# Performance work log

Measured on AMD Instinct MI355X. Metric: run time of the kernel, lower is better.

Reference implementation:

```python
import jax, jax.numpy as jnp
import numpy as np

NUM_SUB = (128, 32)
NUM_NEI = (24, 24)
LN_EPS = 1e-5


def bilinear(fmap, pts):
    # fmap: [C,H,W]; pts: [P,2] as (y,x) normalized to [0,1]; align_corners=True
    C, H, W = fmap.shape
    gy = pts[:, 0] * (H - 1)
    gx = pts[:, 1] * (W - 1)
    y0 = jnp.floor(gy)
    x0 = jnp.floor(gx)
    wy = gy - y0
    wx = gx - x0
    y0i = jnp.clip(y0.astype(jnp.int32), 0, H - 1)
    y1i = jnp.clip(y0i + 1, 0, H - 1)
    x0i = jnp.clip(x0.astype(jnp.int32), 0, W - 1)
    x1i = jnp.clip(x0i + 1, 0, W - 1)
    v00 = fmap[:, y0i, x0i]
    v01 = fmap[:, y0i, x1i]
    v10 = fmap[:, y1i, x0i]
    v11 = fmap[:, y1i, x1i]
    out = (v00 * (1 - wy) * (1 - wx) + v01 * (1 - wy) * wx
           + v10 * wy * (1 - wx) + v11 * wy * wx)
    return out.T  # [P,C]


def fps(xyz, npoint):
    # farthest point sampling, deterministic start at index 0. xyz: [B,N,2]
    B, N, _ = xyz.shape
    bidx = jnp.arange(B)

    def step(carry, _):
        dist, far = carry
        c = xyz[bidx, far][:, None, :]            # [B,1,2]
        d = jnp.sum((xyz - c) ** 2, -1)           # [B,N]
        dist = jnp.minimum(dist, d)
        return (dist, jnp.argmax(dist, -1)), far

    init = (jnp.full((B, N), 1e10, xyz.dtype), jnp.zeros((B,), jnp.int32))
    _, idx = jax.lax.scan(step, init, None, length=npoint)
    return idx.T  # [B,npoint]


def sqdist(a, b):
    # a: [B,S,2], b: [B,N,2] -> [B,S,N]
    return (jnp.sum(a ** 2, -1)[..., None] + jnp.sum(b ** 2, -1)[:, None, :]
            - 2.0 * jnp.einsum('bsc,bnc->bsn', a, b))


def layernorm(x, g, b):
    m = jnp.mean(x, -1, keepdims=True)
    v = jnp.mean((x - m) ** 2, -1, keepdims=True)
    return (x - m) / jnp.sqrt(v + LN_EPS) * g + b


def setup_inputs() -> dict:
    key = jax.random.key(0)
    ks = jax.random.split(key, 8)
    B, N, C, H, W = 32, 512, 1024, 24, 24
    Dp = C + 2
    out_dim = 4096
    return {
        'feature_map': jax.random.normal(ks[0], (B, C, H, W), jnp.float32),
        'points': jax.random.uniform(ks[1], (B, N, 2), jnp.float32),
        'W_diff': jax.random.normal(ks[2], (2, Dp, Dp), jnp.float32) * 0.02,
        'b_diff': jnp.zeros((2, Dp), jnp.float32),
        'W_agg': jax.random.normal(ks[3], (2, C, 2 * Dp), jnp.float32) * 0.02,
        'b_agg': jnp.zeros((2, C), jnp.float32),
        'ln_g': jnp.ones((2, C), jnp.float32),
        'ln_b': jnp.zeros((2, C), jnp.float32),
        'W_flat': jax.random.normal(ks[4], (C, C * NUM_SUB[-1]), jnp.float32) * 0.02,
        'b_flat': jnp.zeros((C,), jnp.float32),
        'W_dim': jax.random.normal(ks[5], (out_dim, C), jnp.float32) * 0.02,
        'b_dim': jnp.zeros((out_dim,), jnp.float32),
    }


def reference(feature_map, points, W_diff, b_diff, W_agg, b_agg,
              ln_g, ln_b, W_flat, b_flat, W_dim, b_dim):
    B = points.shape[0]
    all_pts = points                              # [B,N,2]
    all_fea = jax.vmap(bilinear)(feature_map, points)  # [B,N,C]
    bidx = jnp.arange(B)[:, None, None]
    for i, (S, K) in enumerate(zip(NUM_SUB, NUM_NEI)):
        fi = fps(all_pts, S)                                   # [B,S]
        new_pts = jnp.take_along_axis(all_pts, fi[..., None], 1)   # [B,S,2]
        new_fea = jnp.take_along_axis(all_fea, fi[..., None], 1)   # [B,S,C]
        d2 = sqdist(new_pts, all_pts)                          # [B,S,N]
        _, idx = jax.lax.top_k(-d2, K)                         # [B,S,K]
        grp_pts = all_pts[bidx, idx]                           # [B,S,K,2]
        grp_fea = all_fea[bidx, idx]                           # [B,S,K,C]
        local = jnp.concatenate([grp_fea, grp_pts], -1)        # [B,S,K,C+2]
        anchor = jnp.concatenate([new_fea, new_pts], -1)[:, :, None, :]
        diff = jnp.einsum('bskd,od->bsko', local - anchor, W_diff[i]) + b_diff[i]
        gath = jnp.concatenate([diff, jnp.broadcast_to(anchor, diff.shape)], -1)
        # Conv1d(kernel=1) + ReLU + LayerNorm over channels
        h = jax.nn.relu(jnp.einsum('bskd,od->bsko', gath, W_agg[i]) + b_agg[i])
        h = layernorm(h, ln_g[i], ln_b[i])
        all_pts, all_fea = new_pts, jnp.mean(h, 2)             # mean pool over K
    x = all_fea.reshape(B, -1)
    x = x @ W_flat.T + b_flat
    return x @ W_dim.T + b_dim
```

## Files before the change

### kernel.cpp

```cpp
#include <hip/hip_runtime.h>


typedef float f32x4 __attribute__((ext_vector_type(4)));
typedef short bf16x8 __attribute__((ext_vector_type(8)));
typedef unsigned short u16;
typedef u16 u16x4 __attribute__((ext_vector_type(4)));
typedef unsigned int u32;
typedef u32 u32x4 __attribute__((ext_vector_type(4)));
typedef unsigned long long u64;

typedef const void __attribute__((address_space(1)))* gvp;
typedef void __attribute__((address_space(3)))* svp;

__device__ __forceinline__ u16 f2bf(float f) {
  union { float f; u32 u; } x; x.f = f;
  u32 r = x.u + 0x7fffu + ((x.u >> 16) & 1u);
  return (u16)(r >> 16);
}

#define KP 1056
#define NP0 1152

__device__ __forceinline__ float rl_f(float v, int lane) {
  return __int_as_float(__builtin_amdgcn_readlane(__float_as_int(v), lane));
}

template <int CTRL>
__device__ __forceinline__ float dpp_fmax(float v) {
  float o = __int_as_float(__builtin_amdgcn_update_dpp(
      (int)0xff800000 , __float_as_int(v), CTRL, 0xf, 0xf, false));
  return fmaxf(v, o);
}

template <int CTRL>
__device__ __forceinline__ float dpp_fmin(float v) {
  float o = __int_as_float(__builtin_amdgcn_update_dpp(
      0x7f800000 , __float_as_int(v), CTRL, 0xf, 0xf, false));
  return fminf(v, o);
}

template <int CTRL>
__device__ __forceinline__ float dpp_add(float v) {
  float o = __int_as_float(__builtin_amdgcn_update_dpp(
      0, __float_as_int(v), CTRL, 0xf, 0xf, false));
  return v + o;
}

__device__ __forceinline__ float wave_fmax63(float v) {
  v = dpp_fmax<0x111>(v);
  v = dpp_fmax<0x112>(v);
  v = dpp_fmax<0x114>(v);
  v = dpp_fmax<0x118>(v);
  v = dpp_fmax<0x142>(v);
  v = dpp_fmax<0x143>(v);
  return rl_f(v, 63);
}

__device__ __forceinline__ float wave_fmin63(float v) {
  v = dpp_fmin<0x111>(v);
  v = dpp_fmin<0x112>(v);
  v = dpp_fmin<0x114>(v);
  v = dpp_fmin<0x118>(v);
  v = dpp_fmin<0x142>(v);
  v = dpp_fmin<0x143>(v);
  return rl_f(v, 63);
}

__device__ __forceinline__ float wave_sum63(float v) {
  v = dpp_add<0x111>(v);
  v = dpp_add<0x112>(v);
  v = dpp_add<0x114>(v);
  v = dpp_add<0x118>(v);
  v = dpp_add<0x142>(v);
  v = dpp_add<0x143>(v);
  return v;
}

template <int PPL, int HS>
__device__ void fps_core(const float* __restrict__ pts, int* __restrict__ fi,
                         float* __restrict__ npts,
                         int Np, int S, int b, int lane, int s0, int s1,
                         float* __restrict__ dsave, int* __restrict__ fsave) {
  #pragma clang fp contract(off)
  float px[PPL], py[PPL], dist[PPL];
  #pragma unroll
  for (int j = 0; j < PPL; ++j) {
    int n = j * 64 + lane;
    px[j] = pts[((size_t)b * Np + n) * 2];
    py[j] = pts[((size_t)b * Np + n) * 2 + 1];
  }
  int far; float cx, cy;
  if (s0 == 0) {
    #pragma unroll
    for (int j = 0; j < PPL; ++j) dist[j] = 1e10f;
    far = 0;
    cx = rl_f(px[0], 0);
    cy = rl_f(py[0], 0);
  } else {
    #pragma unroll
    for (int j = 0; j < PPL; ++j) dist[j] = dsave[(size_t)b * Np + j * 64 + lane];
    far = fsave[b];
    cx = pts[((size_t)b * Np + far) * 2];
    cy = pts[((size_t)b * Np + far) * 2 + 1];
  }
  int hist[HS];
  #pragma unroll
  for (int h = 0; h < HS; ++h) hist[h] = 0;
  for (int s = s0; s < s1; ++s) {
    #pragma unroll
    for (int h = 0; h < HS; ++h)
      if ((s >> 6) == h && (s & 63) == lane) hist[h] = far;
    float tv[PPL]; int ti[PPL]; float tx[PPL], ty[PPL];
    #pragma unroll
    for (int j = 0; j < PPL; ++j) {
      float dx = px[j] - cx, dy = py[j] - cy;
      float d = dx * dx + dy * dy;
      float nd = fminf(dist[j], d);
      dist[j] = nd;
      tv[j] = nd; ti[j] = j * 64 + lane; tx[j] = px[j]; ty[j] = py[j];
    }
    #pragma unroll
    for (int w = PPL; w > 1; w >>= 1)
      #pragma unroll
      for (int j = 0; j < (w >> 1); ++j)
        if (tv[j + (w >> 1)] > tv[j]) {
          tv[j] = tv[j + (w >> 1)]; ti[j] = ti[j + (w >> 1)];
          tx[j] = tx[j + (w >> 1)]; ty[j] = ty[j + (w >> 1)];
        }
    float smax = wave_fmax63(tv[0]);
    u64 mask = __ballot(tv[0] == smax);
    int L = __builtin_ctzll(mask);
    int fidx = __builtin_amdgcn_readlane(ti[0], L);
    float fx = rl_f(tx[0], L), fy = rl_f(ty[0], L);
    u64 rest = mask & (mask - 1);
    if (__builtin_expect(rest != 0, 0)) {
      while (rest) {
        int L2 = __builtin_ctzll(rest);
        int c = __builtin_amdgcn_readlane(ti[0], L2);
        if (c < fidx) {
          fidx = c; fx = rl_f(tx[0], L2); fy = rl_f(ty[0], L2);
        }
        rest &= rest - 1;
      }
    }
    far = fidx; cx = fx; cy = fy;
  }
  if (s1 < S) {
    #pragma unroll
    for (int j = 0; j < PPL; ++j) dsave[(size_t)b * Np + j * 64 + lane] = dist[j];
    if (lane == 0) fsave[b] = far;
  }
  #pragma unroll
  for (int h = 0; h < HS; ++h) {
    int s = h * 64 + lane;
    if (s >= s0 && s < s1) {
      int hv = hist[h];
      fi[b * S + s] = hv;
      npts[(size_t)(b * S + s) * 2]     = pts[((size_t)b * Np + hv) * 2];
      npts[(size_t)(b * S + s) * 2 + 1] = pts[((size_t)b * Np + hv) * 2 + 1];
    }
  }
}

template <int PPL>
__device__ void knn_core(const float* __restrict__ qpts,
                         const float* __restrict__ rpts,
                         int* __restrict__ idxK, int Np, int S, int q, int lane) {
  #pragma clang fp contract(off)
  int b = q / S;
  float ax = qpts[(size_t)q * 2], ay = qpts[(size_t)q * 2 + 1];
  float a2 = ax * ax + ay * ay;
  float d2[PPL];
  #pragma unroll
  for (int j = 0; j < PPL; ++j) {
    int n = j * 64 + lane;
    float bx = rpts[((size_t)b * Np + n) * 2];
    float by = rpts[((size_t)b * Np + n) * 2 + 1];
    float b2 = bx * bx + by * by;
    float dot = ax * bx + ay * by;
    float t = a2 + b2;
    float m2 = 2.f * dot;
    d2[j] = t - m2;
  }
  int kreg = 0;
  for (int k = 0; k < 24; ++k) {
    float tv[PPL]; int ti[PPL];
    #pragma unroll
    for (int j = 0; j < PPL; ++j) { tv[j] = d2[j]; ti[j] = j * 64 + lane; }
    #pragma unroll
    for (int w = PPL; w > 1; w >>= 1)
      #pragma unroll
      for (int j = 0; j < (w >> 1); ++j)
        if (tv[j + (w >> 1)] < tv[j]) {
          tv[j] = tv[j + (w >> 1)]; ti[j] = ti[j + (w >> 1)];
        }
    float smin = wave_fmin63(tv[0]);
    u64 mask = __ballot(tv[0] == smin);
    int L = __builtin_ctzll(mask);
    int bs = __builtin_amdgcn_readlane(ti[0], L);
    u64 rest = mask & (mask - 1);
    if (__builtin_expect(rest != 0, 0)) {
      while (rest) {
        int L2 = __builtin_ctzll(rest);
        int c = __builtin_amdgcn_readlane(ti[0], L2);
        if (c < bs) bs = c;
        rest &= rest - 1;
      }
    }
    if (lane == k) kreg = bs;
    #pragma unroll
    for (int j = 0; j < PPL; ++j)
      if (j * 64 + lane == bs) d2[j] = 3.4e38f;
  }
  if (lane < 24) idxK[(size_t)q * 24 + lane] = kreg;
}

template <int BF16OUT, int IND>
__device__ __forceinline__ void gemm_tile_body(const u16* __restrict__ A,
                                               const u16* __restrict__ Bt,
                                               void* __restrict__ Cout,
                                               int K, int ldc, int nvalid,
                                               int m0, int n0,
                                               const int* __restrict__ find,
                                               int iNp, int iS,
                                               u16* __restrict__ As,
                                               u16* __restrict__ Bs) {
  const int tid = threadIdx.x;
  const int lane = tid & 63;
  const int wv = tid >> 6;
  const int wm = (wv >> 1) * 64;
  const int wn = (wv & 1) * 64;

  f32x4 acc[4][4];
  #pragma unroll
  for (int i = 0; i < 4; ++i)
    #pragma unroll
    for (int j = 0; j < 4; ++j)
      #pragma unroll
      for (int c = 0; c < 4; ++c) acc[i][j][c] = 0.f;

  const int ch0 = wv * 2;
  const int rin = lane >> 2;
  const int slot = lane & 3;
  const int cin = (slot ^ (rin & 3) ^ ((rin >> 2) & 3)) * 8;

  size_t aro[2];
  #pragma unroll
  for (int i = 0; i < 2; ++i) {
    const int row = (ch0 + i) * 16 + rin;
    if (IND) {
      const int q = m0 + row;
      aro[i] = (size_t)(q / iS) * iNp + find[q];
    } else {
      aro[i] = (size_t)(m0 + row);
    }
  }

  for (int k0 = 0; k0 < K; k0 += 32) {
    #pragma unroll
    for (int i = 0; i < 2; ++i) {
      const int ch = ch0 + i;
      const int row = ch * 16 + rin;
      const u16* ga = A + aro[i] * K + (k0 + cin);
      const u16* gb = Bt + (size_t)(n0 + row) * K + (k0 + cin);
      __builtin_amdgcn_global_load_lds((gvp)ga, (svp)(As + ch * 512), 16, 0, 0);
      __builtin_amdgcn_global_load_lds((gvp)gb, (svp)(Bs + ch * 512), 16, 0, 0);
    }
    __syncthreads();
    const int rf = lane & 15;
    const int quad = lane >> 4;
    const int qs = (quad ^ (rf & 3) ^ ((rf >> 2) & 3)) * 8;
    bf16x8 af[4], bfv[4];
    #pragma unroll
    for (int mi = 0; mi < 4; ++mi)
      af[mi] = *(const bf16x8*)(As + (wm + mi * 16 + rf) * 32 + qs);
    #pragma unroll
    for (int ni = 0; ni < 4; ++ni)
      bfv[ni] = *(const bf16x8*)(Bs + (wn + ni * 16 + rf) * 32 + qs);
    #pragma unroll
    for (int mi = 0; mi < 4; ++mi)
      #pragma unroll
      for (int ni = 0; ni < 4; ++ni)
        acc[mi][ni] = __builtin_amdgcn_mfma_f32_16x16x32_bf16(af[mi], bfv[ni], acc[mi][ni], 0, 0, 0);
    __syncthreads();
  }

  const int rq = (lane >> 4) * 4;
  const int cf = lane & 15;
  #pragma unroll
  for (int mi = 0; mi < 4; ++mi) {
    #pragma unroll
    for (int ni = 0; ni < 4; ++ni) {
      const int col = n0 + wn + ni * 16 + cf;
      #pragma unroll
      for (int r = 0; r < 4; ++r) {
        const int row = m0 + wm + mi * 16 + rq + r;
        const float v = acc[mi][ni][r];
        if (BF16OUT) {
          if (col < nvalid) ((u16*)Cout)[(size_t)row * ldc + col] = f2bf(v);
        } else {
          ((float*)Cout)[(size_t)row * ldc + col] = v;
        }
      }
    }
  }
}

__global__ __launch_bounds__(256, 2) void bilinear_fused_kernel(const float* __restrict__ fmap,
                                                                const float* __restrict__ pts,
                                                                u16* __restrict__ X,
                                                                int* __restrict__ fi0,
                                                                float* __restrict__ npts0,
                                                                float* __restrict__ fdist,
                                                                int* __restrict__ ffar) {
  if (blockIdx.y == 0) {
    if (blockIdx.x < 8)
      fps_core<8, 2>(pts, fi0, npts0, 512, 128, blockIdx.x * 4 + (threadIdx.x >> 6),
                     threadIdx.x & 63, 0, 32, fdist, ffar);
    return;
  }
  __shared__ float fmS[32][580];
  const int ct = blockIdx.x, b = blockIdx.y - 1;
  const int t = threadIdx.x;
  const float* src = fmap + ((size_t)b * 1024 + ct * 32) * 576;
  const int tr = t >> 3, ti = t & 7;
  #pragma unroll
  for (int j = 0; j < 18; ++j) {
    int c4 = j * 8 + ti;
    *(f32x4*)&fmS[tr][c4 * 4] = *(const f32x4*)(src + (size_t)tr * 576 + c4 * 4);
  }
  __syncthreads();
  #pragma unroll
  for (int pass = 0; pass < 2; ++pass) {
    const int n = pass * 256 + t;
    const int pidx = b * 512 + n;
    float p0 = pts[(size_t)pidx * 2], p1 = pts[(size_t)pidx * 2 + 1];
    float gy = p0 * 23.f, gx = p1 * 23.f;
    float y0f = floorf(gy), x0f = floorf(gx);
    float wy = gy - y0f, wx = gx - x0f;
    int y0 = (int)y0f; y0 = y0 < 0 ? 0 : (y0 > 23 ? 23 : y0);
    int x0 = (int)x0f; x0 = x0 < 0 ? 0 : (x0 > 23 ? 23 : x0);
    int y1 = y0 + 1 > 23 ? 23 : y0 + 1;
    int x1 = x0 + 1 > 23 ? 23 : x0 + 1;
    float w00 = (1.f - wy) * (1.f - wx), w01 = (1.f - wy) * wx;
    float w10 = wy * (1.f - wx), w11 = wy * wx;
    const int i00 = y0 * 24 + x0, i01 = y0 * 24 + x1;
    const int i10 = y1 * 24 + x0, i11 = y1 * 24 + x1;
    size_t ro = (size_t)pidx * KP + ct * 32;
    #pragma unroll
    for (int cq = 0; cq < 8; ++cq) {
      u16x4 o4;
      #pragma unroll
      for (int cc = 0; cc < 4; ++cc) {
        int c = cq * 4 + cc;
        float v = w00 * fmS[c][i00] + w01 * fmS[c][i01] +
                  w10 * fmS[c][i10] + w11 * fmS[c][i11];
        o4[cc] = f2bf(v);
      }
      *(u16x4*)(X + ro + cq * 4) = o4;
    }
    if (ct == 31) {
      size_t rb = (size_t)pidx * KP;
      X[rb + 1024] = f2bf(p0);
      X[rb + 1025] = f2bf(p1);
      #pragma unroll
      for (int z = 0; z < 15; ++z) ((u32*)(X + rb + 1026))[z] = 0;
    }
  }
}

__global__ __launch_bounds__(256) void wd_transpose_kernel(const float* __restrict__ Wd,
                                                           u16* __restrict__ WdT) {
  __shared__ float tbuf[32][33];
  const float* Wds = Wd + (size_t)blockIdx.z * 1026 * 1026;
  u16* WdTs = WdT + (size_t)blockIdx.z * NP0 * KP;
  int tx = threadIdx.x & 31, ty = threadIdx.x >> 5;
  int ot = blockIdx.x * 32, dt = blockIdx.y * 32;
  #pragma unroll
  for (int j = 0; j < 4; ++j) {
    int o = ot + ty + 8 * j, d = dt + tx;
    tbuf[ty + 8 * j][tx] = (o < 1026 && d < 1026) ? Wds[(size_t)o * 1026 + d] : 0.f;
  }
  __syncthreads();
  #pragma unroll
  for (int j = 0; j < 4; ++j) {
    int d = dt + ty + 8 * j, o = ot + tx;
    if (o < KP) WdTs[(size_t)d * KP + o] = f2bf(tbuf[tx][ty + 8 * j]);
  }
}

__global__ __launch_bounds__(256) void waggcz_kernel(const float* __restrict__ Wagg,
                                                     const float* __restrict__ bdiff,
                                                     const float* __restrict__ bagg,
                                                     u16* __restrict__ Wa1,
                                                     u16* __restrict__ Wa2,
                                                     float* __restrict__ czero) {
  __shared__ float red[4];
  const int bid = blockIdx.x;
  const int stage = bid >> 10, c = bid & 1023;
  const float* row = Wagg + (size_t)stage * 1024 * 2052 + (size_t)c * 2052;
  const float* bd = bdiff + stage * 1026;
  u16* wa1 = Wa1 + (size_t)stage * 1024 * KP + (size_t)c * KP;
  u16* wa2 = Wa2 + (size_t)stage * 1024 * KP + (size_t)c * KP;
  const int t = threadIdx.x;
  float acc = 0.f;
  for (int d = t; d < KP; d += 256) {
    if (d < 1026) {
      float v1 = row[d];
      float v2 = row[1026 + d];
      wa1[d] = f2bf(v1);
      wa2[d] = f2bf(v2);
      acc += bd[d] * v1;
    } else {
      wa1[d] = 0;
      wa2[d] = 0;
    }
  }
  float s = wave_sum63(acc);
  const int lane = t & 63, wv = t >> 6;
  if (lane == 63) red[wv] = s;
  __syncthreads();
  if (t == 0)
    czero[(size_t)stage * 1024 + c] = red[0] + red[1] + red[2] + red[3] + bagg[stage * 1024 + c];
}

__global__ __launch_bounds__(256) void wcomb_dual_kernel(const u16* __restrict__ Wa1,
                                                         const u16* __restrict__ WdT,
                                                         u16* __restrict__ Wcomb,
                                                         const float* __restrict__ fpts,
                                                         int* __restrict__ ffi,
                                                         float* __restrict__ fnpts,
                                                         float* __restrict__ fdist,
                                                         int* __restrict__ ffar) {
  __shared__ __align__(16) u16 As[128 * 32];
  __shared__ __align__(16) u16 Bs[128 * 32];
  const int wv = threadIdx.x >> 6, lane = threadIdx.x & 63;
  if (blockIdx.y == 0) {
    if (blockIdx.x < 8)
      fps_core<8, 2>(fpts, ffi, fnpts, 512, 128, blockIdx.x * 4 + wv, lane, 32, 56,
                     fdist, ffar);
    return;
  }
  const int y = blockIdx.y - 1;
  const int stage = y >> 3;
  const int mt = y & 7;
  const u16* A = Wa1 + (size_t)stage * 1024 * KP;
  const u16* B = WdT + (size_t)stage * NP0 * KP;
  u16* C = Wcomb + (size_t)stage * 1024 * KP;
  gemm_tile_body<1, 0>(A, B, C, KP, KP, KP, mt * 128, blockIdx.x * 128,
                       nullptr, 0, 0, As, Bs);
}

template <int BF16OUT, int FPS_PPL, int FPS_HS, int SWZ, int KNN_PPL, int IND>
__global__ __launch_bounds__(256) void gemm_bt_kernel(const u16* __restrict__ A,
                                                      const u16* __restrict__ Bt,
                                                      void* __restrict__ Cout,
                                                      int K, int ldc, int nvalid,
                                                      const int* __restrict__ find,
                                                      int iNp, int iS,
                                                      const float* __restrict__ fpts,
                                                      int* __restrict__ ffi,
                                                      float* __restrict__ fnpts,
                                                      int fNp, int fS, int fs0, int fs1,
                                                      float* __restrict__ fdist,
                                                      int* __restrict__ ffar,
                                                      const float* __restrict__ kq,
                                                      const float* __restrict__ kr,
                                                      int* __restrict__ kidx,
                                                      int kNp, int kS, int kYoff) {
  const int tid = threadIdx.x;
  const int lane = tid & 63;
  const int wv = tid >> 6;
  const int FR = (FPS_PPL > 0) ? 1 : 0;
  if (FPS_PPL > 0 && blockIdx.y == 0) {
    if (blockIdx.x < 8)
      fps_core<FPS_PPL ? FPS_PPL : 1, FPS_HS>(fpts, ffi, fnpts, fNp, fS,
                                              blockIdx.x * 4 + wv, lane, fs0, fs1,
                                              fdist, ffar);
    return;
  }
  if (KNN_PPL > 0 && (int)blockIdx.y >= kYoff) {
    int kb = ((int)blockIdx.y - kYoff) * gridDim.x + blockIdx.x;
    knn_core<KNN_PPL ? KNN_PPL : 1>(kq, kr, kidx, kNp, kS, kb * 4 + wv, lane);
    return;
  }
  __shared__ __align__(16) u16 As[128 * 32];
  __shared__ __align__(16) u16 Bs[128 * 32];
  int mt, nt;
  if (SWZ) {
    const int g = ((int)blockIdx.y - FR) * gridDim.x + blockIdx.x;
    const int MT = (KNN_PPL > 0 ? kYoff : (int)gridDim.y) - FR;
    const int cpx = MT >> 3;
    const int xcd = g & 7;
    const int r = g >> 3;
    mt = xcd * cpx + (r >> 3);
    nt = r & 7;
  } else {
    mt = (int)blockIdx.y - FR;
    nt = blockIdx.x;
  }
  gemm_tile_body<BF16OUT, IND>(A, Bt, Cout, K, ldc, nvalid, mt * 128, nt * 128,
                               find, iNp, iS, As, Bs);
}

template <int MODE, int FPS_PPL, int FPS_HS>
__global__ __launch_bounds__(256) void h_epilogue_kernel(const float* __restrict__ Z1,
                                                         const float* __restrict__ Z2g,
                                                         const float* __restrict__ czero,
                                                         const int* __restrict__ idxK,
                                                         const int* __restrict__ fi,
                                                         const float* __restrict__ g,
                                                         const float* __restrict__ bb,
                                                         const float* __restrict__ npts,
                                                         void* __restrict__ outp,
                                                         int Np, int S, int cpx,
                                                         const float* __restrict__ fpts,
                                                         int* __restrict__ ffi,
                                                         float* __restrict__ fnpts,
                                                         int fNp, int fS) {
  const int t = threadIdx.x;
  const int lane = t & 63, wv = t >> 6;
  if (FPS_PPL > 0 && blockIdx.x < 8) {
    fps_core<FPS_PPL ? FPS_PPL : 1, FPS_HS>(fpts, ffi, fnpts, fNp, fS,
                                            blockIdx.x * 4 + wv, lane, 0, fS,
                                            nullptr, nullptr);
    return;
  }
  const int bid = blockIdx.x - (FPS_PPL > 0 ? 8 : 0);
  const int sw = (bid & 7) * cpx + (bid >> 3);
  const int q = sw * 4 + wv;
  const int b = q / S;
  const int fiv = fi[q];
  const float* z2 = Z2g + (size_t)q * 1024;
  const float* zf = Z1 + ((size_t)b * Np + fiv) * 1024;
  const int ch = lane * 4;

  f32x4 base[4], gv[4], bv[4], acc[4];
  #pragma unroll
  for (int j = 0; j < 4; ++j) {
    f32x4 a = *(const f32x4*)(z2 + j * 256 + ch);
    f32x4 c = *(const f32x4*)(czero + j * 256 + ch);
    f32x4 f = *(const f32x4*)(zf + j * 256 + ch);
    #pragma unroll
    for (int c2 = 0; c2 < 4; ++c2) base[j][c2] = a[c2] + c[c2] - f[c2];
    gv[j] = *(const f32x4*)(g + j * 256 + ch);
    bv[j] = *(const f32x4*)(bb + j * 256 + ch);
    #pragma unroll
    for (int c2 = 0; c2 < 4; ++c2) acc[j][c2] = 0.f;
  }
  int nk = 0;
  if (lane < 24) nk = idxK[(size_t)q * 24 + lane];

  for (int k = 0; k < 24; ++k) {
    const int n = __builtin_amdgcn_readlane(nk, k);
    const float* zr = Z1 + ((size_t)b * Np + n) * 1024;
    f32x4 v[4];
    float s1 = 0.f, s2 = 0.f;
    #pragma unroll
    for (int j = 0; j < 4; ++j) {
      f32x4 r = *(const f32x4*)(zr + j * 256 + ch);
      #pragma unroll
      for (int c2 = 0; c2 < 4; ++c2) {
        float x = fmaxf(r[c2] + base[j][c2], 0.f);
        v[j][c2] = x;
        s1 += x;
        s2 += x * x;
      }
    }
    s1 = wave_sum63(s1);
    s2 = wave_sum63(s2);
    const float S1 = rl_f(s1, 63);
    const float S2 = rl_f(s2, 63);
    const float m = S1 * (1.f / 1024.f);
    const float var = S2 * (1.f / 1024.f) - m * m;
    const float rs = rsqrtf(var + 1e-5f);
    #pragma unroll
    for (int j = 0; j < 4; ++j)
      #pragma unroll
      for (int c2 = 0; c2 < 4; ++c2)
        acc[j][c2] += (v[j][c2] - m) * rs * gv[j][c2] + bv[j][c2];
  }

  u16x4 o4[4];
  #pragma unroll
  for (int j = 0; j < 4; ++j)
    #pragma unroll
    for (int c2 = 0; c2 < 4; ++c2) o4[j][c2] = f2bf(acc[j][c2] * (1.f / 24.f));

  if (MODE == 0) {
    u16* X = (u16*)outp;
    size_t ro = (size_t)q * KP;
    #pragma unroll
    for (int j = 0; j < 4; ++j) *(u16x4*)(X + ro + j * 256 + ch) = o4[j];
    if (lane == 0) {
      X[ro + 1024] = f2bf(npts[(size_t)q * 2]);
      X[ro + 1025] = f2bf(npts[(size_t)q * 2 + 1]);
    }
    if (lane < 15) ((u32*)(X + ro + 1026))[lane] = 0;
  } else {
    u16* X = (u16*)outp + (size_t)q * 1024;
    #pragma unroll
    for (int j = 0; j < 4; ++j) *(u16x4*)(X + j * 256 + ch) = o4[j];
  }
}

template <int KSBITS, int NST>
__global__ __launch_bounds__(256, 4) void mlp_mfma_kernel(const float* __restrict__ W,
                                                          const u16* __restrict__ Fb,
                                                          float* __restrict__ P, int K) {
  __shared__ __align__(16) float Asf[128 * 32];
  __shared__ __align__(16) u16 Fsb[32 * 40];
  const int tid = threadIdx.x, lane = tid & 63, wv = tid >> 6;
  const int ot = blockIdx.x >> KSBITS;
  const int ks = blockIdx.x & ((1 << KSBITS) - 1);
  const int m0 = ot * 128;
  const int k0b = ks * (NST * 32);
  const int arow = lane >> 3;
  const int agrp = lane & 7;
  const int rf = lane & 15, quad = lane >> 4;

  f32x4 acc[2][2];
  #pragma unroll
  for (int i = 0; i < 2; ++i)
    #pragma unroll
    for (int j = 0; j < 2; ++j)
      #pragma unroll
      for (int c = 0; c < 4; ++c) acc[i][j][c] = 0.f;

  for (int st = 0; st < NST; ++st) {
    const int k0 = k0b + st * 32;
    #pragma unroll
    for (int i = 0; i < 4; ++i) {
      const int row = wv * 32 + i * 8 + arow;
      const int g = agrp ^ (row & 7);
      const float* ga = W + (size_t)(m0 + row) * K + k0 + g * 4;
      __builtin_amdgcn_global_load_lds((gvp)ga, (svp)(Asf + (wv * 32 + i * 8) * 32), 16, 0, 0);
    }
    if (tid < 128) {
      const int fr = tid >> 2, fc = (tid & 3) * 8;
      u32x4 tmp = *(const u32x4*)(Fb + (size_t)fr * K + k0 + fc);
      *(u32x4*)(Fsb + fr * 40 + fc) = tmp;
    }
    __syncthreads();
    bf16x8 bfr[2];
    #pragma unroll
    for (int ni = 0; ni < 2; ++ni)
      bfr[ni] = *(const bf16x8*)(Fsb + (ni * 16 + rf) * 40 + quad * 8);
    #pragma unroll
    for (int mi = 0; mi < 2; ++mi) {
      const float* ap = Asf + (size_t)(wv * 32 + mi * 16 + rf) * 32;
      f32x4 a0 = *(const f32x4*)(ap + (((quad * 2) ^ (rf & 7)) * 4));
      f32x4 a1 = *(const f32x4*)(ap + (((quad * 2 + 1) ^ (rf & 7)) * 4));
      union { bf16x8 v; u16 h[8]; } af;
      #pragma unroll
      for (int c = 0; c < 4; ++c) { af.h[c] = f2bf(a0[c]); af.h[4 + c] = f2bf(a1[c]); }
      #pragma unroll
      for (int ni = 0; ni < 2; ++ni)
        acc[mi][ni] = __builtin_amdgcn_mfma_f32_16x16x32_bf16(af.v, bfr[ni], acc[mi][ni], 0, 0, 0);
    }
    __syncthreads();
  }

  float* Pb = P + (size_t)blockIdx.x * 4096;
  const int rq = (lane >> 4) * 4, cf = lane & 15;
  #pragma unroll
  for (int mi = 0; mi < 2; ++mi)
    #pragma unroll
    for (int ni = 0; ni < 2; ++ni)
      #pragma unroll
      for (int r = 0; r < 4; ++r)
        Pb[(wv * 32 + mi * 16 + rq + r) * 32 + ni * 16 + cf] = acc[mi][ni][r];
}

__global__ __launch_bounds__(256) void reduce_flat_kernel(const float* __restrict__ P,
                                                          const float* __restrict__ bias,
                                                          u16* __restrict__ x1bf) {
  int idx = blockIdx.x * 256 + threadIdx.x;
  int o = idx >> 5, b = idx & 31;
  float s = bias[o];
  const float* p = P + ((size_t)(o >> 7) * 64) * 4096 + (o & 127) * 32 + b;
  #pragma unroll 8
  for (int ks = 0; ks < 64; ++ks) s += p[(size_t)ks * 4096];
  x1bf[(size_t)b * 1024 + o] = f2bf(s);
}

__global__ __launch_bounds__(256) void reduce_dim_kernel(const float* __restrict__ P,
                                                         const float* __restrict__ bias,
                                                         float* __restrict__ out) {
  int idx = blockIdx.x * 256 + threadIdx.x;
  int o = idx >> 5, b = idx & 31;
  float s = bias[o];
  const float* p = P + ((size_t)(o >> 7) * 8) * 4096 + (o & 127) * 32 + b;
  #pragma unroll
  for (int ks = 0; ks < 8; ++ks) s += p[(size_t)ks * 4096];
  out[(size_t)b * 4096 + o] = s;
}

extern "C" void kernel_launch(void* const* d_in, const int* in_sizes, int n_in,
                              void* d_out, int out_size, void* d_ws, size_t ws_size,
                              hipStream_t stream) {
  const float* fmap  = (const float*)d_in[0];
  const float* pts   = (const float*)d_in[1];
  const float* Wdiff = (const float*)d_in[2];
  const float* bdiff = (const float*)d_in[3];
  const float* Wagg  = (const float*)d_in[4];
  const float* bagg  = (const float*)d_in[5];
  const float* lng   = (const float*)d_in[6];
  const float* lnb   = (const float*)d_in[7];
  const float* Wflat = (const float*)d_in[8];
  const float* bflat = (const float*)d_in[9];
  const float* Wdim  = (const float*)d_in[10];
  const float* bdim  = (const float*)d_in[11];
  float* out = (float*)d_out;

  char* w = (char*)d_ws;
  size_t off = 0;
  auto alloc = [&](size_t n) { char* p = w + off; off += (n + 255) & ~(size_t)255; return p; };

  float* Z1    = (float*)alloc(16384ull * 1024 * 4);
  float* Z2g   = (float*)alloc(4096ull * 1024 * 4);
  u16* Xbf0  = (u16*)alloc(16384ull * KP * 2);
  u16* X1bf  = (u16*)alloc(4096ull * KP * 2);
  u16* WdT   = (u16*)alloc(2ull * NP0 * KP * 2);
  u16* Wa1   = (u16*)alloc(2ull * 1024 * KP * 2);
  u16* Wa2   = (u16*)alloc(2ull * 1024 * KP * 2);
  u16* Wcomb = (u16*)alloc(2ull * 1024 * KP * 2);
  float* czero = (float*)alloc(2 * 1024 * 4);
  int* fi0   = (int*)alloc(32 * 128 * 4);
  int* fi1   = (int*)alloc(32 * 32 * 4);
  int* idx0  = (int*)alloc(32 * 128 * 24 * 4);
  int* idx1  = (int*)alloc(32 * 32 * 24 * 4);
  float* npts0 = (float*)alloc(32 * 128 * 2 * 4);
  float* npts1 = (float*)alloc(32 * 32 * 2 * 4);
  u16* fea2bf = (u16*)alloc(32ull * 32768 * 2);
  u16* x1bf   = (u16*)alloc(32ull * 1024 * 2);
  float* Pf   = (float*)alloc(512ull * 4096 * 4);
  float* Pd   = (float*)alloc(256ull * 4096 * 4);
  float* fdist = (float*)alloc(32ull * 512 * 4);
  int* ffar    = (int*)alloc(32 * 4);

  bilinear_fused_kernel<<<dim3(32, 33), 256, 0, stream>>>(fmap, pts, Xbf0, fi0, npts0,
                                                          fdist, ffar);
  wd_transpose_kernel<<<dim3(33, 36, 2), 256, 0, stream>>>(Wdiff, WdT);
  waggcz_kernel<<<2048, 256, 0, stream>>>(Wagg, bdiff, bagg, Wa1, Wa2, czero);
  wcomb_dual_kernel<<<dim3(9, 17), 256, 0, stream>>>(Wa1, WdT, Wcomb, pts, fi0, npts0,
                                                     fdist, ffar);
  gemm_bt_kernel<0, 8, 2, 1, 0, 0><<<dim3(8, 129), 256, 0, stream>>>(
      Xbf0, Wcomb, Z1, KP, 1024, 1024,
      nullptr, 0, 0,
      pts, fi0, npts0, 512, 128, 56, 128, fdist, ffar,
      nullptr, nullptr, nullptr, 0, 0, 0);
  gemm_bt_kernel<0, 0, 1, 1, 8, 1><<<dim3(8, 160), 256, 0, stream>>>(
      Xbf0, Wa2, Z2g, KP, 1024, 1024,
      fi0, 512, 128,
      nullptr, nullptr, nullptr, 0, 0, 0, 0, nullptr, nullptr,
      npts0, pts, idx0, 512, 128, 32);
  h_epilogue_kernel<0, 2, 1><<<1032, 256, 0, stream>>>(
      Z1, Z2g, czero, idx0, fi0, lng, lnb, npts0, X1bf, 512, 128, 128,
      npts0, fi1, npts1, 128, 32);
  gemm_bt_kernel<0, 0, 1, 1, 0, 0><<<dim3(8, 32), 256, 0, stream>>>(
      X1bf, Wcomb + 1024ull * KP, Z1, KP, 1024, 1024,
      nullptr, 0, 0,
      nullptr, nullptr, nullptr, 0, 0, 0, 0, nullptr, nullptr,
      nullptr, nullptr, nullptr, 0, 0, 0);
  gemm_bt_kernel<0, 0, 1, 1, 2, 1><<<dim3(8, 40), 256, 0, stream>>>(
      X1bf, Wa2 + 1024ull * KP, Z2g, KP, 1024, 1024,
      fi1, 128, 32,
      nullptr, nullptr, nullptr, 0, 0, 0, 0, nullptr, nullptr,
      npts1, npts0, idx1, 128, 32, 8);
  h_epilogue_kernel<1, 0, 1><<<256, 256, 0, stream>>>(
      Z1, Z2g, czero + 1024, idx1, fi1, lng + 1024, lnb + 1024, npts1, fea2bf,
      128, 32, 32, nullptr, nullptr, nullptr, 0, 0);

  mlp_mfma_kernel<6, 16><<<512, 256, 0, stream>>>(Wflat, fea2bf, Pf, 32768);
  reduce_flat_kernel<<<128, 256, 0, stream>>>(Pf, bflat, x1bf);
  mlp_mfma_kernel<3, 4><<<256, 256, 0, stream>>>(Wdim, x1bf, Pd, 1024);
  reduce_dim_kernel<<<512, 256, 0, stream>>>(Pd, bdim, out);
}
```

Measured before the change: 551.4 us.

## Merge prep kernels, fuse stage-1 GEMMs with kNN, pre-convert W_flat to bf16

Merges the W_diff transpose and W_agg conversion into one launch that also hosts the first slice of farthest point sampling. The sampling steps are redistributed across kernels. The Z1 GEMM kernel gains blocks that convert the fp32 W_flat matrix to bf16 while the GEMM runs. The final MLP then reads half the bytes through a new bf16 MFMA kernel that loads weights with global_load_lds. The two stage-1 GEMMs and their kNN are fused into one launch to cut launch count and tail idle time. In exchange, the 128 MB W_flat still has to be converted every call, which adds a separate read and write pass.

```diff
diff --git a/kernel.cpp b/kernel.cpp
--- a/kernel.cpp
+++ b/kernel.cpp
@@ -369,40 +369,56 @@
   }
 }
 
-__global__ __launch_bounds__(256) void wd_transpose_kernel(const float* __restrict__ Wd,
-                                                           u16* __restrict__ WdT) {
+__global__ __launch_bounds__(256) void prep_merged_kernel(const float* __restrict__ Wd,
+                                                          u16* __restrict__ WdT,
+                                                          const float* __restrict__ Wagg,
+                                                          const float* __restrict__ bdiff,
+                                                          const float* __restrict__ bagg,
+                                                          u16* __restrict__ Wa1,
+                                                          u16* __restrict__ Wa2,
+                                                          float* __restrict__ czero,
+                                                          const float* __restrict__ fpts,
+                                                          int* __restrict__ ffi,
+                                                          float* __restrict__ fnpts,
+                                                          float* __restrict__ fdist,
+                                                          int* __restrict__ ffar) {
   __shared__ float tbuf[32][33];
-  const float* Wds = Wd + (size_t)blockIdx.z * 1026 * 1026;
-  u16* WdTs = WdT + (size_t)blockIdx.z * NP0 * KP;
-  int tx = threadIdx.x & 31, ty = threadIdx.x >> 5;
-  int ot = blockIdx.x * 32, dt = blockIdx.y * 32;
-  #pragma unroll
-  for (int j = 0; j < 4; ++j) {
-    int o = ot + ty + 8 * j, d = dt + tx;
-    tbuf[ty + 8 * j][tx] = (o < 1026 && d < 1026) ? Wds[(size_t)o * 1026 + d] : 0.f;
-  }
-  __syncthreads();
-  #pragma unroll
-  for (int j = 0; j < 4; ++j) {
-    int d = dt + ty + 8 * j, o = ot + tx;
-    if (o < KP) WdTs[(size_t)d * KP + o] = f2bf(tbuf[tx][ty + 8 * j]);
-  }
-}
-
-__global__ __launch_bounds__(256) void waggcz_kernel(const float* __restrict__ Wagg,
-                                                     const float* __restrict__ bdiff,
-                                                     const float* __restrict__ bagg,
-                                                     u16* __restrict__ Wa1,
-                                                     u16* __restrict__ Wa2,
-                                                     float* __restrict__ czero) {
   __shared__ float red[4];
   const int bid = blockIdx.x;
-  const int stage = bid >> 10, c = bid & 1023;
+  const int t = threadIdx.x;
+  const int lane = t & 63, wv = t >> 6;
+  if (bid < 8) {
+    fps_core<8, 2>(fpts, ffi, fnpts, 512, 128, bid * 4 + wv, lane, 32, 56, fdist, ffar);
+    return;
+  }
+  if (bid < 8 + 2376) {
+    const int i = bid - 8;
+    const int z = i / 1188;
+    const int r = i % 1188;
+    const int bx = r % 33, by = r / 33;
+    const float* Wds = Wd + (size_t)z * 1026 * 1026;
+    u16* WdTs = WdT + (size_t)z * NP0 * KP;
+    int tx = t & 31, ty = t >> 5;
+    int ot = bx * 32, dt = by * 32;
+    #pragma unroll
+    for (int j = 0; j < 4; ++j) {
+      int o = ot + ty + 8 * j, d = dt + tx;
+      tbuf[ty + 8 * j][tx] = (o < 1026 && d < 1026) ? Wds[(size_t)o * 1026 + d] : 0.f;
+    }
+    __syncthreads();
+    #pragma unroll
+    for (int j = 0; j < 4; ++j) {
+      int d = dt + ty + 8 * j, o = ot + tx;
+      if (o < KP) WdTs[(size_t)d * KP + o] = f2bf(tbuf[tx][ty + 8 * j]);
+    }
+    return;
+  }
+  const int i = bid - (8 + 2376);
+  const int stage = i >> 10, c = i & 1023;
   const float* row = Wagg + (size_t)stage * 1024 * 2052 + (size_t)c * 2052;
   const float* bd = bdiff + stage * 1026;
   u16* wa1 = Wa1 + (size_t)stage * 1024 * KP + (size_t)c * KP;
   u16* wa2 = Wa2 + (size_t)stage * 1024 * KP + (size_t)c * KP;
-  const int t = threadIdx.x;
   float acc = 0.f;
   for (int d = t; d < KP; d += 256) {
     if (d < 1026) {
@@ -417,7 +433,6 @@
     }
   }
   float s = wave_sum63(acc);
-  const int lane = t & 63, wv = t >> 6;
   if (lane == 63) red[wv] = s;
   __syncthreads();
   if (t == 0)
@@ -437,7 +452,7 @@
   const int wv = threadIdx.x >> 6, lane = threadIdx.x & 63;
   if (blockIdx.y == 0) {
     if (blockIdx.x < 8)
-      fps_core<8, 2>(fpts, ffi, fnpts, 512, 128, blockIdx.x * 4 + wv, lane, 32, 56,
+      fps_core<8, 2>(fpts, ffi, fnpts, 512, 128, blockIdx.x * 4 + wv, lane, 56, 78,
                      fdist, ffar);
     return;
   }
@@ -451,19 +466,58 @@
                        nullptr, 0, 0, As, Bs);
 }
 
-template <int BF16OUT, int FPS_PPL, int FPS_HS, int SWZ, int KNN_PPL, int IND>
+__global__ __launch_bounds__(256) void z1_fused_kernel(const u16* __restrict__ A,
+                                                       const u16* __restrict__ Bt,
+                                                       float* __restrict__ C,
+                                                       const float* __restrict__ Wflat,
+                                                       u16* __restrict__ WflatBf,
+                                                       const float* __restrict__ fpts,
+                                                       int* __restrict__ ffi,
+                                                       float* __restrict__ fnpts,
+                                                       float* __restrict__ fdist,
+                                                       int* __restrict__ ffar) {
+  const int t = threadIdx.x;
+  const int lane = t & 63, wv = t >> 6;
+  if (blockIdx.y == 0) {
+    if (blockIdx.x < 8)
+      fps_core<8, 2>(fpts, ffi, fnpts, 512, 128, blockIdx.x * 4 + wv, lane, 78, 128,
+                     fdist, ffar);
+    return;
+  }
+  if (blockIdx.y < 33) {
+    const int cb = ((int)blockIdx.y - 1) * 8 + blockIdx.x;
+    const f32x4* src = (const f32x4*)Wflat;
+    u16x4* dst = (u16x4*)WflatBf;
+    int idx = cb * 256 + t;
+    #pragma unroll 4
+    for (int it = 0; it < 128; ++it) {
+      f32x4 v = src[idx];
+      u16x4 o;
+      #pragma unroll
+      for (int c = 0; c < 4; ++c) o[c] = f2bf(v[c]);
+      dst[idx] = o;
+      idx += 65536;
+    }
+    return;
+  }
+  __shared__ __align__(16) u16 As[128 * 32];
+  __shared__ __align__(16) u16 Bs[128 * 32];
+  const int g = ((int)blockIdx.y - 33) * 8 + blockIdx.x;
+  const int xcd = g & 7;
+  const int r = g >> 3;
+  const int mt = xcd * 16 + (r >> 3);
+  const int nt = r & 7;
+  gemm_tile_body<0, 0>(A, Bt, C, KP, 1024, 1024, mt * 128, nt * 128,
+                       nullptr, 0, 0, As, Bs);
+}
+
+template <int BF16OUT, int SWZ, int KNN_PPL, int IND>
 __global__ __launch_bounds__(256) void gemm_bt_kernel(const u16* __restrict__ A,
                                                       const u16* __restrict__ Bt,
                                                       void* __restrict__ Cout,
                                                       int K, int ldc, int nvalid,
                                                       const int* __restrict__ find,
                                                       int iNp, int iS,
-                                                      const float* __restrict__ fpts,
-                                                      int* __restrict__ ffi,
-                                                      float* __restrict__ fnpts,
-                                                      int fNp, int fS, int fs0, int fs1,
-                                                      float* __restrict__ fdist,
-                                                      int* __restrict__ ffar,
                                                       const float* __restrict__ kq,
                                                       const float* __restrict__ kr,
                                                       int* __restrict__ kidx,
@@ -471,14 +525,6 @@
   const int tid = threadIdx.x;
   const int lane = tid & 63;
   const int wv = tid >> 6;
-  const int FR = (FPS_PPL > 0) ? 1 : 0;
-  if (FPS_PPL > 0 && blockIdx.y == 0) {
-    if (blockIdx.x < 8)
-      fps_core<FPS_PPL ? FPS_PPL : 1, FPS_HS>(fpts, ffi, fnpts, fNp, fS,
-                                              blockIdx.x * 4 + wv, lane, fs0, fs1,
-                                              fdist, ffar);
-    return;
-  }
   if (KNN_PPL > 0 && (int)blockIdx.y >= kYoff) {
     int kb = ((int)blockIdx.y - kYoff) * gridDim.x + blockIdx.x;
     knn_core<KNN_PPL ? KNN_PPL : 1>(kq, kr, kidx, kNp, kS, kb * 4 + wv, lane);
@@ -488,19 +534,52 @@
   __shared__ __align__(16) u16 Bs[128 * 32];
   int mt, nt;
   if (SWZ) {
-    const int g = ((int)blockIdx.y - FR) * gridDim.x + blockIdx.x;
-    const int MT = (KNN_PPL > 0 ? kYoff : (int)gridDim.y) - FR;
+    const int g = (int)blockIdx.y * gridDim.x + blockIdx.x;
+    const int MT = (KNN_PPL > 0 ? kYoff : (int)gridDim.y);
     const int cpx = MT >> 3;
     const int xcd = g & 7;
     const int r = g >> 3;
     mt = xcd * cpx + (r >> 3);
     nt = r & 7;
   } else {
-    mt = (int)blockIdx.y - FR;
+    mt = (int)blockIdx.y;
     nt = blockIdx.x;
   }
   gemm_tile_body<BF16OUT, IND>(A, Bt, Cout, K, ldc, nvalid, mt * 128, nt * 128,
                                find, iNp, iS, As, Bs);
+}
+
+__global__ __launch_bounds__(256) void stage1_fused_kernel(const u16* __restrict__ X1bf,
+                                                           const u16* __restrict__ Wcomb1,
+                                                           const u16* __restrict__ Wa21,
+                                                           float* __restrict__ Z1,
+                                                           float* __restrict__ Z2g,
+                                                           const int* __restrict__ fi1,
+                                                           const float* __restrict__ npts1,
+                                                           const float* __restrict__ npts0,
+                                                           int* __restrict__ idx1) {
+  __shared__ __align__(16) u16 As[128 * 32];
+  __shared__ __align__(16) u16 Bs[128 * 32];
+  const int lane = threadIdx.x & 63, wv = threadIdx.x >> 6;
+  if (blockIdx.y < 32) {
+    const int g = (int)blockIdx.y * 8 + blockIdx.x;
+    const int xcd = g & 7;
+    const int r = g >> 3;
+    const int mt = xcd * 4 + (r >> 3);
+    const int nt = r & 7;
+    gemm_tile_body<0, 0>(X1bf, Wcomb1, Z1, KP, 1024, 1024, mt * 128, nt * 128,
+                         nullptr, 0, 0, As, Bs);
+    return;
+  }
+  if (blockIdx.y < 40) {
+    const int mt = (int)blockIdx.y - 32;
+    const int nt = blockIdx.x;
+    gemm_tile_body<0, 1>(X1bf, Wa21, Z2g, KP, 1024, 1024, mt * 128, nt * 128,
+                         fi1, 128, 32, As, Bs);
+    return;
+  }
+  const int kb = ((int)blockIdx.y - 40) * 8 + blockIdx.x;
+  knn_core<2>(npts1, npts0, idx1, 128, 32, kb * 4 + wv, lane);
 }
 
 template <int MODE, int FPS_PPL, int FPS_HS>
@@ -605,6 +684,70 @@
 }
 
 template <int KSBITS, int NST>
+__global__ __launch_bounds__(256, 4) void mlp_mfma_bf16_kernel(const u16* __restrict__ W,
+                                                               const u16* __restrict__ Fb,
+                                                               float* __restrict__ P, int K) {
+  __shared__ __align__(16) u16 As[128 * 32];
+  __shared__ __align__(16) u16 Fsb[32 * 40];
+  const int tid = threadIdx.x, lane = tid & 63, wv = tid >> 6;
+  const int ot = blockIdx.x >> KSBITS;
+  const int ks = blockIdx.x & ((1 << KSBITS) - 1);
+  const int m0 = ot * 128;
+  const int k0b = ks * (NST * 32);
+  const int rin = lane >> 2;
+  const int slot = lane & 3;
+  const int cin = (slot ^ (rin & 3) ^ ((rin >> 2) & 3)) * 8;
+  const int rf = lane & 15, quad = lane >> 4;
+  const int qs = (quad ^ (rf & 3) ^ ((rf >> 2) & 3)) * 8;
+
+  f32x4 acc[2][2];
+  #pragma unroll
+  for (int i = 0; i < 2; ++i)
+    #pragma unroll
+    for (int j = 0; j < 2; ++j)
+      #pragma unroll
+      for (int c = 0; c < 4; ++c) acc[i][j][c] = 0.f;
+
+  for (int st = 0; st < NST; ++st) {
+    const int k0 = k0b + st * 32;
+    #pragma unroll
+    for (int i = 0; i < 2; ++i) {
+      const int row = wv * 32 + i * 16 + rin;
+      const u16* ga = W + (size_t)(m0 + row) * K + k0 + cin;
+      __builtin_amdgcn_global_load_lds((gvp)ga, (svp)(As + (wv * 32 + i * 16) * 32), 16, 0, 0);
+    }
+    if (tid < 128) {
+      const int fr = tid >> 2, fc = (tid & 3) * 8;
+      u32x4 tmp = *(const u32x4*)(Fb + (size_t)fr * K + k0 + fc);
+      *(u32x4*)(Fsb + fr * 40 + fc) = tmp;
+    }
+    __syncthreads();
+    bf16x8 bfr[2];
+    #pragma unroll
+    for (int ni = 0; ni < 2; ++ni)
+      bfr[ni] = *(const bf16x8*)(Fsb + (ni * 16 + rf) * 40 + quad * 8);
+    #pragma unroll
+    for (int mi = 0; mi < 2; ++mi) {
+      bf16x8 af = *(const bf16x8*)(As + (wv * 32 + mi * 16 + rf) * 32 + qs);
+      #pragma unroll
+      for (int ni = 0; ni < 2; ++ni)
+        acc[mi][ni] = __builtin_amdgcn_mfma_f32_16x16x32_bf16(af, bfr[ni], acc[mi][ni], 0, 0, 0);
+    }
+    __syncthreads();
+  }
+
+  float* Pb = P + (size_t)blockIdx.x * 4096;
+  const int rq = (lane >> 4) * 4, cf = lane & 15;
+  #pragma unroll
+  for (int mi = 0; mi < 2; ++mi)
+    #pragma unroll
+    for (int ni = 0; ni < 2; ++ni)
+      #pragma unroll
+      for (int r = 0; r < 4; ++r)
+        Pb[(wv * 32 + mi * 16 + rq + r) * 32 + ni * 16 + cf] = acc[mi][ni][r];
+}
+
+template <int KSBITS, int NST>
 __global__ __launch_bounds__(256, 4) void mlp_mfma_kernel(const float* __restrict__ W,
                                                           const u16* __restrict__ Fb,
                                                           float* __restrict__ P, int K) {
@@ -725,6 +868,7 @@
   u16* Wa1   = (u16*)alloc(2ull * 1024 * KP * 2);
   u16* Wa2   = (u16*)alloc(2ull * 1024 * KP * 2);
   u16* Wcomb = (u16*)alloc(2ull * 1024 * KP * 2);
+  u16* WflatBf = (u16*)alloc(1024ull * 32768 * 2);
   float* czero = (float*)alloc(2 * 1024 * 4);
   int* fi0   = (int*)alloc(32 * 128 * 4);
   int* fi1   = (int*)alloc(32 * 32 * 4);
@@ -741,38 +885,28 @@
 
   bilinear_fused_kernel<<<dim3(32, 33), 256, 0, stream>>>(fmap, pts, Xbf0, fi0, npts0,
                                                           fdist, ffar);
-  wd_transpose_kernel<<<dim3(33, 36, 2), 256, 0, stream>>>(Wdiff, WdT);
-  waggcz_kernel<<<2048, 256, 0, stream>>>(Wagg, bdiff, bagg, Wa1, Wa2, czero);
+  prep_merged_kernel<<<4432, 256, 0, stream>>>(Wdiff, WdT, Wagg, bdiff, bagg,
+                                               Wa1, Wa2, czero, pts, fi0, npts0,
+                                               fdist, ffar);
   wcomb_dual_kernel<<<dim3(9, 17), 256, 0, stream>>>(Wa1, WdT, Wcomb, pts, fi0, npts0,
                                                      fdist, ffar);
-  gemm_bt_kernel<0, 8, 2, 1, 0, 0><<<dim3(8, 129), 256, 0, stream>>>(
-      Xbf0, Wcomb, Z1, KP, 1024, 1024,
-      nullptr, 0, 0,
-      pts, fi0, npts0, 512, 128, 56, 128, fdist, ffar,
-      nullptr, nullptr, nullptr, 0, 0, 0);
-  gemm_bt_kernel<0, 0, 1, 1, 8, 1><<<dim3(8, 160), 256, 0, stream>>>(
+  z1_fused_kernel<<<dim3(8, 161), 256, 0, stream>>>(Xbf0, Wcomb, Z1, Wflat, WflatBf,
+                                                    pts, fi0, npts0, fdist, ffar);
+  gemm_bt_kernel<0, 1, 8, 1><<<dim3(8, 160), 256, 0, stream>>>(
       Xbf0, Wa2, Z2g, KP, 1024, 1024,
       fi0, 512, 128,
-      nullptr, nullptr, nullptr, 0, 0, 0, 0, nullptr, nullptr,
       npts0, pts, idx0, 512, 128, 32);
   h_epilogue_kernel<0, 2, 1><<<1032, 256, 0, stream>>>(
       Z1, Z2g, czero, idx0, fi0, lng, lnb, npts0, X1bf, 512, 128, 128,
       npts0, fi1, npts1, 128, 32);
-  gemm_bt_kernel<0, 0, 1, 1, 0, 0><<<dim3(8, 32), 256, 0, stream>>>(
-      X1bf, Wcomb + 1024ull * KP, Z1, KP, 1024, 1024,
-      nullptr, 0, 0,
-      nullptr, nullptr, nullptr, 0, 0, 0, 0, nullptr, nullptr,
-      nullptr, nullptr, nullptr, 0, 0, 0);
-  gemm_bt_kernel<0, 0, 1, 1, 2, 1><<<dim3(8, 40), 256, 0, stream>>>(
-      X1bf, Wa2 + 1024ull * KP, Z2g, KP, 1024, 1024,
-      fi1, 128, 32,
-      nullptr, nullptr, nullptr, 0, 0, 0, 0, nullptr, nullptr,
-      npts1, npts0, idx1, 128, 32, 8);
+  stage1_fused_kernel<<<dim3(8, 72), 256, 0, stream>>>(
+      X1bf, Wcomb + 1024ull * KP, Wa2 + 1024ull * KP, Z1, Z2g, fi1,
+      npts1, npts0, idx1);
   h_epilogue_kernel<1, 0, 1><<<256, 256, 0, stream>>>(
       Z1, Z2g, czero + 1024, idx1, fi1, lng + 1024, lnb + 1024, npts1, fea2bf,
       128, 32, 32, nullptr, nullptr, nullptr, 0, 0);
 
-  mlp_mfma_kernel<6, 16><<<512, 256, 0, stream>>>(Wflat, fea2bf, Pf, 32768);
+  mlp_mfma_bf16_kernel<6, 16><<<512, 256, 0, stream>>>(WflatBf, fea2bf, Pf, 32768);
   reduce_flat_kernel<<<128, 256, 0, stream>>>(Pf, bflat, x1bf);
   mlp_mfma_kernel<3, 4><<<256, 256, 0, stream>>>(Wdim, x1bf, Pd, 1024);
   reduce_dim_kernel<<<512, 256, 0, stream>>>(Pd, bdim, out);
```

Result: slower. 574.2 us (+4.1%).
